# Kernel tuning notes

Hardware: AMD Instinct MI355X
Metric: run time of the kernel (lower is better)

The kernel has to match this reference:

```python
import jax, jax.numpy as jnp
import numpy as np
from jax import lax

VDECAY = 0.5
VTH = 0.5
GRAD_WIN = 0.5

B, IN_DIM, T = 128, 2048, 32
H = 2048
OUT = 512

@jax.custom_vjp
def spike(v):
    return (v > VTH).astype(v.dtype)

def _spike_fwd(v):
    return spike(v), v

def _spike_bwd(v, g):
    # rectangular surrogate gradient (PseudoSpikeRect)
    return (g * (jnp.abs(v - VTH) < GRAD_WIN).astype(g.dtype),)

spike.defvjp(_spike_fwd, _spike_bwd)

def setup_inputs() -> dict:
    key = jax.random.key(0)
    ks = jax.random.split(key, 4)
    scale = 1.0 / np.sqrt(2048)
    return {
        "spike_data": (jax.random.uniform(ks[0], (B, IN_DIM, T)) < 0.3).astype(jnp.float32),
        "h0_volt": jnp.zeros((B, H), jnp.float32),
        "h0_spike": jnp.zeros((B, H), jnp.float32),
        "h1_volt": jnp.zeros((B, H), jnp.float32),
        "h1_spike": jnp.zeros((B, H), jnp.float32),
        "o_volt": jnp.zeros((B, OUT), jnp.float32),
        "o_spike": jnp.zeros((B, OUT), jnp.float32),
        "W0": jax.random.normal(ks[1], (H, IN_DIM), jnp.float32) * scale,
        "b0": jnp.zeros((H,), jnp.float32),
        "W1": jax.random.normal(ks[2], (H, H), jnp.float32) * scale,
        "b1": jnp.zeros((H,), jnp.float32),
        "Wo": jax.random.normal(ks[3], (OUT, H), jnp.float32) * scale,
        "bo": jnp.zeros((OUT,), jnp.float32),
        "batch_size": B,
        "spike_ts": T,
    }

def _lif(x, volt, spk, W, b):
    # volt decays only where no spike occurred (soft reset via (1 - spike))
    volt = VDECAY * volt * (1.0 - spk) + x @ W.T + b
    new_spk = spike(volt)
    return new_spk, volt

def reference(spike_data, h0_volt, h0_spike, h1_volt, h1_spike, o_volt, o_spike,
              W0, b0, W1, b1, Wo, bo, batch_size, spike_ts):
    x = spike_data.reshape(batch_size, -1, spike_ts)
    xt = jnp.transpose(x, (2, 0, 1))  # [T, B, in_dim]

    def step(carry, inp):
        (v0, s0), (v1, s1), (vo, so) = carry
        s0, v0 = _lif(inp, v0, s0, W0, b0)
        s1, v1 = _lif(s0, v1, s1, W1, b1)
        so, vo = _lif(s1, vo, so, Wo, bo)
        return ((v0, s0), (v1, s1), (vo, so)), so

    carry0 = ((h0_volt, h0_spike), (h1_volt, h1_spike), (o_volt, o_spike))
    _, out_spikes = lax.scan(step, carry0, xt)  # [T, B, OUT]
    return out_spikes.sum(axis=0)
```

## Files before the change

### kernel.cpp

```cpp
#include <hip/hip_runtime.h>
#include <cstdint>

#define B_   128
#define T_   32
#define IN_  2048
#define H_   2048
#define OUT_ 512

typedef __attribute__((address_space(1))) const void* gas_cp;
typedef __attribute__((address_space(3))) void* las_p;

__global__ __launch_bounds__(256) void k_transpose(const float* __restrict__ in,
                                                   float* __restrict__ Xt) {
    int idx = blockIdx.x * 256 + threadIdx.x;
    int b = idx >> 11;
    int i = idx & (IN_ - 1);
    const float4* p = (const float4*)(in + (size_t)idx * T_);
#pragma unroll
    for (int q = 0; q < 8; ++q) {
        float4 v = p[q];
        int t = q * 4;
        Xt[((size_t)((t + 0) * B_ + b) << 11) + i] = v.x;
        Xt[((size_t)((t + 1) * B_ + b) << 11) + i] = v.y;
        Xt[((size_t)((t + 2) * B_ + b) << 11) + i] = v.z;
        Xt[((size_t)((t + 3) * B_ + b) << 11) + i] = v.w;
    }
}

__global__ __launch_bounds__(256)
void k_gemm_seq(const float* __restrict__ A, const float* __restrict__ W,
                float* __restrict__ C, int M, int N, int K) {
    constexpr int BM = 64, BN = 128, BK = 32;
    constexpr int NT = 8;
    constexpr int BUFF = (BM + BN) * BK;
    __shared__ alignas(16) float lds[2][BUFF];

    const int tid = threadIdx.x;
    const int tx  = tid & 15;
    const int ty  = tid >> 4;
    const int m0  = blockIdx.y * BM;
    const int n0  = blockIdx.x * BN;
    const int w   = tid >> 6;

    const float* srcA[2];
    int dstA[2];
#pragma unroll
    for (int q = 0; q < 2; ++q) {
        int L = q * 256 + tid;
        int r = L >> 3;
        int s = ((L & 7) - ((r + (r >> 4)) & 7)) & 7;
        srcA[q] = A + (size_t)(m0 + r) * K + s * 4;
        dstA[q] = q * 1024 + w * 256;
    }
    const float* srcW[4];
    int dstW[4];
#pragma unroll
    for (int q = 0; q < 4; ++q) {
        int L = q * 256 + tid;
        int r = L >> 3;
        int s = ((L & 7) - ((r + (r >> 4)) & 7)) & 7;
        srcW[q] = W + (size_t)(n0 + r) * K + s * 4;
        dstW[q] = BM * BK + q * 1024 + w * 256;
    }

    float acc[4][NT];
    float tot[4][NT];
#pragma unroll
    for (int i = 0; i < 4; ++i)
#pragma unroll
        for (int j = 0; j < NT; ++j) { acc[i][j] = 0.0f; tot[i][j] = 0.0f; }

    const int nkt = K / BK;

#pragma unroll
    for (int q = 0; q < 2; ++q) {
        __builtin_amdgcn_global_load_lds((gas_cp)srcA[q], (las_p)&lds[0][dstA[q]], 16, 0, 0);
        srcA[q] += BK;
    }
#pragma unroll
    for (int q = 0; q < 4; ++q) {
        __builtin_amdgcn_global_load_lds((gas_cp)srcW[q], (las_p)&lds[0][dstW[q]], 16, 0, 0);
        srcW[q] += BK;
    }

    int cur = 0;
    for (int kt = 0; kt < nkt; ++kt) {
        __syncthreads();

        if (kt + 1 < nkt) {
            int nb = cur ^ 1;
#pragma unroll
            for (int q = 0; q < 2; ++q) {
                __builtin_amdgcn_global_load_lds((gas_cp)srcA[q], (las_p)&lds[nb][dstA[q]], 16, 0, 0);
                srcA[q] += BK;
            }
#pragma unroll
            for (int q = 0; q < 4; ++q) {
                __builtin_amdgcn_global_load_lds((gas_cp)srcW[q], (las_p)&lds[nb][dstW[q]], 16, 0, 0);
                srcW[q] += BK;
            }
        }

        const float* At = &lds[cur][0];
        const float* Wt = &lds[cur][BM * BK];

#pragma unroll
        for (int gk = 0; gk < 8; ++gk) {
            float4 av[4], wv[NT];
#pragma unroll
            for (int i = 0; i < 4; ++i) {
                int r = ty + 16 * i;
                int rot = (r + (r >> 4)) & 7;
                av[i] = *(const float4*)&At[r * BK + (((gk + rot) & 7) << 2)];
            }
#pragma unroll
            for (int j = 0; j < NT; ++j) {
                int r = tx + 16 * j;
                int rot = (r + (r >> 4)) & 7;
                wv[j] = *(const float4*)&Wt[r * BK + (((gk + rot) & 7) << 2)];
            }
#pragma unroll
            for (int q = 0; q < 4; ++q)
#pragma unroll
                for (int i = 0; i < 4; ++i)
#pragma unroll
                    for (int j = 0; j < NT; ++j)
                        acc[i][j] = __builtin_fmaf(((const float*)&av[i])[q],
                                                   ((const float*)&wv[j])[q],
                                                   acc[i][j]);
        }

        if (((kt + 1) & 15) == 0) {
#pragma unroll
            for (int i = 0; i < 4; ++i)
#pragma unroll
                for (int j = 0; j < NT; ++j) {
                    tot[i][j] = tot[i][j] + acc[i][j];
                    acc[i][j] = 0.0f;
                }
        }
        cur ^= 1;
    }

#pragma unroll
    for (int i = 0; i < 4; ++i)
#pragma unroll
        for (int j = 0; j < NT; ++j)
            C[(size_t)(m0 + ty + 16 * i) * N + (n0 + tx + 16 * j)] = tot[i][j];
}

__global__ __launch_bounds__(256) void k_scan_h(const float* __restrict__ Acc,
                                                const float* __restrict__ v_init,
                                                const float* __restrict__ s_init,
                                                const float* __restrict__ bias,
                                                float* __restrict__ Sout) {
    int idx = blockIdx.x * 256 + threadIdx.x;
    int h = idx & (H_ - 1);
    float v = v_init[idx];
    float s = s_init[idx];
    float bb = bias[h];
#pragma unroll
    for (int t = 0; t < T_; ++t) {
        float x = Acc[(size_t)t * (B_ * H_) + idx];
        float d = 0.5f * v;
        d = d * (1.0f - s);
        v = d + x;
        v = v + bb;
        s = (v > 0.5f) ? 1.0f : 0.0f;
        Sout[(size_t)t * (B_ * H_) + idx] = s;
    }
}

__global__ __launch_bounds__(256) void k_scan_o(const float* __restrict__ Acc,
                                                const float* __restrict__ v_init,
                                                const float* __restrict__ s_init,
                                                const float* __restrict__ bias,
                                                float* __restrict__ out) {
    int idx = blockIdx.x * 256 + threadIdx.x;
    int o = idx & (OUT_ - 1);
    float v = v_init[idx];
    float s = s_init[idx];
    float bb = bias[o];
    float acc = 0.0f;
#pragma unroll
    for (int t = 0; t < T_; ++t) {
        float x = Acc[(size_t)t * (B_ * OUT_) + idx];
        float d = 0.5f * v;
        d = d * (1.0f - s);
        v = d + x;
        v = v + bb;
        s = (v > 0.5f) ? 1.0f : 0.0f;
        acc += s;
    }
    out[idx] = acc;
}


extern "C" void kernel_launch(void* const* d_in, const int* in_sizes, int n_in,
                              void* d_out, int out_size, void* d_ws, size_t ws_size,
                              hipStream_t stream) {
    const float* spike_data = (const float*)d_in[0];
    const float* h0_volt  = (const float*)d_in[1];
    const float* h0_spike = (const float*)d_in[2];
    const float* h1_volt  = (const float*)d_in[3];
    const float* h1_spike = (const float*)d_in[4];
    const float* o_volt   = (const float*)d_in[5];
    const float* o_spike  = (const float*)d_in[6];
    const float* W0 = (const float*)d_in[7];
    const float* b0 = (const float*)d_in[8];
    const float* W1 = (const float*)d_in[9];
    const float* b1 = (const float*)d_in[10];
    const float* Wo = (const float*)d_in[11];
    const float* bo = (const float*)d_in[12];
    float* out = (float*)d_out;

    char* ws = (char*)d_ws;
    const size_t MB = (size_t)1 << 20;
    float* Xt = (float*)(ws);
    float* S0 = (float*)(ws + 32 * MB);
    float* Ab = (float*)(ws + 64 * MB);
    float* S1 = Xt;

    const int M = T_ * B_;

    k_transpose<<<(B_ * IN_) / 256, 256, 0, stream>>>(spike_data, Xt);

    k_gemm_seq<<<dim3(H_ / 128, M / 64), 256, 0, stream>>>(Xt, W0, Ab, M, H_, IN_);
    k_scan_h<<<(B_ * H_) / 256, 256, 0, stream>>>(Ab, h0_volt, h0_spike, b0, S0);

    k_gemm_seq<<<dim3(H_ / 128, M / 64), 256, 0, stream>>>(S0, W1, Ab, M, H_, H_);
    k_scan_h<<<(B_ * H_) / 256, 256, 0, stream>>>(Ab, h1_volt, h1_spike, b1, S1);

    k_gemm_seq<<<dim3(OUT_ / 128, M / 64), 256, 0, stream>>>(S1, Wo, Ab, M, OUT_, H_);
    k_scan_o<<<(B_ * OUT_) / 256, 256, 0, stream>>>(Ab, o_volt, o_spike, bo, out);

    (void)in_sizes; (void)n_in; (void)out_size; (void)ws_size;
}
```

Before: 1.291 ms.

## Add 128x128-tile FP32 GEMM with XOR-swizzled LDS for hidden layers

Adds a new GEMM kernel that gives each block a 128x128 output tile with BK=16 and an 8x8 per-thread register tile, in place of the 64x128 tile with 4x8 per thread. Shared-memory rows are laid out with an XOR swizzle. Partial sums are flushed to global memory every 32 K-steps through volatile read-modify-write, replacing the in-register tot array. The aim is more arithmetic per LDS and global load on the two large hidden-layer GEMMs. The cost is higher register pressure, lower occupancy, and extra global traffic from the partial flushes. The kernel hardcodes 128 K-iterations, so it assumes K=2048.

```diff
diff --git a/kernel.cpp b/kernel.cpp
--- a/kernel.cpp
+++ b/kernel.cpp
@@ -1,5 +1,6 @@
 #include <hip/hip_runtime.h>
 #include <cstdint>
+#include <cstddef>
 
 #define B_   128
 #define T_   32
@@ -25,6 +26,155 @@
         Xt[((size_t)((t + 2) * B_ + b) << 11) + i] = v.z;
         Xt[((size_t)((t + 3) * B_ + b) << 11) + i] = v.w;
     }
+}
+
+__global__ __launch_bounds__(256)
+__attribute__((amdgpu_waves_per_eu(2, 3)))
+void k_gemm_128(const float* __restrict__ A, const float* __restrict__ W,
+                float* __restrict__ C, int M, int N, int K) {
+    constexpr int BK = 16;
+    constexpr int BUFF = 4096;
+    __shared__ alignas(16) float lds[2][BUFF];
+
+    const int tid = threadIdx.x;
+    const int tx  = tid & 15;
+    const int ty  = tid >> 4;
+    const int m0  = blockIdx.y * 128;
+    const int n0  = blockIdx.x * 128;
+    const int w   = tid >> 6;
+
+    const float* srcA[2];
+    const float* srcW[2];
+    int dstA[2], dstW[2];
+#pragma unroll
+    for (int q = 0; q < 2; ++q) {
+        int L = q * 256 + tid;
+        int u = L >> 3, c = L & 7;
+        int v = c ^ (u & 7);
+        int r = 2 * u + (v & 1);
+        int s = v >> 1;
+        srcA[q] = A + (size_t)(m0 + r) * K + s * 4;
+        srcW[q] = W + (size_t)(n0 + r) * K + s * 4;
+        dstA[q] = q * 1024 + w * 256;
+        dstW[q] = 2048 + q * 1024 + w * 256;
+    }
+
+    int offA[8], offW[8];
+#pragma unroll
+    for (int i = 0; i < 8; ++i) {
+        int r = ty + 16 * i;
+        int u = r >> 1, y = u & 7;
+        offA[i] = u * 128 + (((r & 1) ^ (y & 1)) << 4) + ((y >> 1) << 5);
+        r = tx + 16 * i;
+        u = r >> 1; y = u & 7;
+        offW[i] = 8192 + u * 128 + (((r & 1) ^ (y & 1)) << 4) + ((y >> 1) << 5);
+    }
+
+    float acc[8][8];
+#pragma unroll
+    for (int i = 0; i < 8; ++i)
+#pragma unroll
+        for (int j = 0; j < 8; ++j) acc[i][j] = 0.0f;
+
+    const char* lbase = (const char*)&lds[0][0];
+    const size_t cb = (size_t)(m0 + ty) * N + (n0 + tx);
+
+#define STAGE(NB)                                                           \
+    {                                                                       \
+        _Pragma("unroll")                                                   \
+        for (int q = 0; q < 2; ++q) {                                       \
+            __builtin_amdgcn_global_load_lds((gas_cp)srcA[q],               \
+                (las_p)&lds[NB][dstA[q]], 16, 0, 0);                        \
+            __builtin_amdgcn_global_load_lds((gas_cp)srcW[q],               \
+                (las_p)&lds[NB][dstW[q]], 16, 0, 0);                        \
+            srcA[q] += BK;                                                  \
+            srcW[q] += BK;                                                  \
+        }                                                                   \
+    }
+
+#define GK4(GKL)                                                            \
+    {                                                                       \
+        float4 wv[8];                                                       \
+        _Pragma("unroll")                                                   \
+        for (int j = 0; j < 8; ++j)                                         \
+            wv[j] = *(const float4*)(lbase + (offW[j] ^ (GKL)));            \
+        {                                                                   \
+            float4 av[4];                                                   \
+            _Pragma("unroll")                                               \
+            for (int i = 0; i < 4; ++i)                                     \
+                av[i] = *(const float4*)(lbase + (offA[i] ^ (GKL)));        \
+            _Pragma("unroll")                                               \
+            for (int q = 0; q < 4; ++q)                                     \
+                _Pragma("unroll")                                           \
+                for (int i = 0; i < 4; ++i)                                 \
+                    _Pragma("unroll")                                       \
+                    for (int j = 0; j < 8; ++j)                             \
+                        acc[i][j] = __builtin_fmaf(((const float*)&av[i])[q], \
+                                                   ((const float*)&wv[j])[q], \
+                                                   acc[i][j]);              \
+        }                                                                   \
+        {                                                                   \
+            float4 av[4];                                                   \
+            _Pragma("unroll")                                               \
+            for (int i = 0; i < 4; ++i)                                     \
+                av[i] = *(const float4*)(lbase + (offA[4 + i] ^ (GKL)));    \
+            _Pragma("unroll")                                               \
+            for (int q = 0; q < 4; ++q)                                     \
+                _Pragma("unroll")                                           \
+                for (int i = 0; i < 4; ++i)                                 \
+                    _Pragma("unroll")                                       \
+                    for (int j = 0; j < 8; ++j)                             \
+                        acc[4 + i][j] = __builtin_fmaf(((const float*)&av[i])[q], \
+                                                       ((const float*)&wv[j])[q], \
+                                                       acc[4 + i][j]);      \
+        }                                                                   \
+    }
+
+    STAGE(0)
+
+    int cur = 0;
+    for (int kt = 0; kt < 128; ++kt) {
+        __syncthreads();
+        if (kt < 127) {
+            int nb = cur ^ 1;
+            STAGE(nb)
+        }
+
+        GK4(0) GK4(32) GK4(64) GK4(96)
+
+        if (((kt + 1) & 31) == 0) {
+            volatile float* Cv = (volatile float*)C;
+            if (kt == 31) {
+#pragma unroll
+                for (int i = 0; i < 8; ++i) {
+                    size_t rowb = cb + (size_t)(i * 16) * N;
+#pragma unroll
+                    for (int j = 0; j < 8; ++j) {
+                        Cv[rowb + j * 16] = acc[i][j];
+                        acc[i][j] = 0.0f;
+                    }
+                }
+            } else {
+#pragma unroll
+                for (int i = 0; i < 8; ++i) {
+                    size_t rowb = cb + (size_t)(i * 16) * N;
+#pragma unroll
+                    for (int j = 0; j < 8; ++j) {
+                        float t = Cv[rowb + j * 16];
+                        Cv[rowb + j * 16] = t + acc[i][j];
+                        acc[i][j] = 0.0f;
+                    }
+                }
+            }
+        }
+
+#pragma unroll
+        for (int i = 0; i < 8; ++i) { offA[i] ^= 16384; offW[i] ^= 16384; }
+        cur ^= 1;
+    }
+
+#undef GK4
+#undef STAGE
 }
 
 __global__ __launch_bounds__(256)
@@ -225,10 +375,10 @@
 
     k_transpose<<<(B_ * IN_) / 256, 256, 0, stream>>>(spike_data, Xt);
 
-    k_gemm_seq<<<dim3(H_ / 128, M / 64), 256, 0, stream>>>(Xt, W0, Ab, M, H_, IN_);
+    k_gemm_128<<<dim3(H_ / 128, M / 128), 256, 0, stream>>>(Xt, W0, Ab, M, H_, IN_);
     k_scan_h<<<(B_ * H_) / 256, 256, 0, stream>>>(Ab, h0_volt, h0_spike, b0, S0);
 
-    k_gemm_seq<<<dim3(H_ / 128, M / 64), 256, 0, stream>>>(S0, W1, Ab, M, H_, H_);
+    k_gemm_128<<<dim3(H_ / 128, M / 128), 256, 0, stream>>>(S0, W1, Ab, M, H_, H_);
     k_scan_h<<<(B_ * H_) / 256, 256, 0, stream>>>(Ab, h1_volt, h1_spike, b1, S1);
 
     k_gemm_seq<<<dim3(OUT_ / 128, M / 64), 256, 0, stream>>>(S1, Wo, Ab, M, OUT_, H_);
```

Result: slower. 1.374 ms (+6.4%).
